# Kernel optimization log

Hardware: AMD Instinct MI355X
Metric: run time of the kernel (lower is better)

## Reference

```python
import jax, jax.numpy as jnp
import numpy as np

DIM = 256      # C
TOPK = 32      # topk_win_num
WIN = 8        # winSize
G = 64         # g (shift group size); 4*G == DIM here


def setup_inputs() -> dict:
    key = jax.random.key(0)
    k0, k1, k2, k3 = jax.random.split(key, 4)
    B, Nt, Ns, C = 32, 256, 4096, DIM
    z = jax.random.normal(k0, (B, Nt, C), jnp.float32)
    x = jax.random.normal(k1, (B, Ns, C), jnp.float32)
    # shift_op_down: Conv2d(C, 4g, 1) -> weight [4g, C]; shift_op_up: Conv2d(4g, C, 1)
    Wd = jax.random.normal(k2, (4 * G, C), jnp.float32) * 0.05
    bd = jnp.zeros((4 * G,), jnp.float32)
    Wu = jax.random.normal(k3, (C, 4 * G), jnp.float32) * 0.05
    bu = jnp.zeros((C,), jnp.float32)
    return {"z": z, "x": x, "Wd": Wd, "bd": bd, "Wu": Wu, "bu": bu}


def reference(z, x, Wd, bd, Wu, bu):
    B, Nt, C = z.shape
    Ns = x.shape[1]
    hs = int(np.sqrt(Ns))
    wn = hs // WIN          # windows per side
    wsa = WIN * WIN         # tokens per window
    K = TOPK

    # AdaptiveMaxPool2d((1,1)) over template tokens -> global max per channel
    z_max = jnp.max(z, axis=1)                               # [B, C]
    sim = jnp.einsum('bc,bnc->bn', z_max, x) / C             # [B, Ns]
    # per-window mean similarity
    sim = sim.reshape(B, wn, WIN, wn, WIN).transpose(0, 1, 3, 2, 4)
    sim = sim.reshape(B, wn * wn, wsa).mean(-1)              # [B, wn*wn]
    idx = jax.lax.top_k(sim, K)[1]                           # [B, K]

    # windowed view of search tokens: [B, wn*wn, wsa, C]
    x_win = x.reshape(B, wn, WIN, wn, WIN, C).transpose(0, 1, 3, 2, 4, 5)
    x_win = x_win.reshape(B, wn * wn, wsa, C)
    x_sel = jnp.take_along_axis(x_win, idx[:, :, None, None], axis=1)  # [B, K, wsa, C]

    xe = x_sel.reshape(B * K, WIN, WIN, C)                   # NHWC per selected window
    t = xe @ Wd.T + bd                                       # 1x1 conv down -> [n, h, w, 4G]

    # 4-direction spatial shift by 1 (zero fill), one channel group per direction
    g0, g1, g2, g3 = t[..., :G], t[..., G:2 * G], t[..., 2 * G:3 * G], t[..., 3 * G:]
    s0 = jnp.pad(g0[:, :, 1:, :], ((0, 0), (0, 0), (0, 1), (0, 0)))  # shift left  (W)
    s1 = jnp.pad(g1[:, :, :-1, :], ((0, 0), (0, 0), (1, 0), (0, 0)))  # shift right (W)
    s2 = jnp.pad(g2[:, 1:, :, :], ((0, 0), (0, 1), (0, 0), (0, 0)))  # shift up    (H)
    s3 = jnp.pad(g3[:, :-1, :, :], ((0, 0), (1, 0), (0, 0), (0, 0)))  # shift down  (H)
    sh = jnp.concatenate([s0, s1, s2, s3], axis=-1)          # [n, h, w, 4G]

    up = sh @ Wu.T + bu                                      # 1x1 conv up -> [n, h, w, C]
    out = (xe + up).reshape(B, K * WIN * WIN, C)             # [B, K*wsa, C]
    return out
```

## Files before the change

kernel.cpp:

```cpp
#include <hip/hip_runtime.h>
#include <hip/hip_bf16.h>

#define C_DIM 256
#define B_SZ 32
#define NS 4096
#define NT_Z 256
#define TOPK_K 32
#define NWIN 64
#define WTOK 64

typedef __attribute__((ext_vector_type(8))) short short8;
typedef __attribute__((ext_vector_type(4))) float f32x4;

static __device__ inline unsigned short f2b(float f) {
  union { float f; unsigned int u; } x; x.f = f;
  unsigned int u = x.u;
  return (unsigned short)((u + 0x7FFFu + ((u >> 16) & 1u)) >> 16);
}
static __device__ inline float b2f(unsigned int h16) {
  union { unsigned int u; float f; } x; x.u = h16 << 16;
  return x.f;
}

__global__ void prep_kernel(const float* __restrict__ Wd, const float* __restrict__ Wu,
                            unsigned short* __restrict__ Wdb, unsigned short* __restrict__ Wub,
                            const float* __restrict__ z, float* __restrict__ zpart) {
  int blk = blockIdx.x;
  if (blk < 64) {
    int i = blk * 256 + threadIdx.x;
    float4 a = ((const float4*)Wd)[i];
    float4 c = ((const float4*)Wu)[i];
    ushort4 ha, hc;
    ha.x = f2b(a.x); ha.y = f2b(a.y); ha.z = f2b(a.z); ha.w = f2b(a.w);
    hc.x = f2b(c.x); hc.y = f2b(c.y); hc.z = f2b(c.z); hc.w = f2b(c.w);
    ((ushort4*)Wdb)[i] = ha;
    ((ushort4*)Wub)[i] = hc;
  } else {
    int i = blk - 64;
    int b = i >> 3, ch = i & 7;
    int c = threadIdx.x;
    const float* p = z + ((size_t)b * NT_Z + ch * 32) * C_DIM + c;
    float m = p[0];
    for (int n = 1; n < 32; ++n) m = fmaxf(m, p[(size_t)n * C_DIM]);
    zpart[(size_t)i * C_DIM + c] = m;
  }
}

__global__ __launch_bounds__(256) void winscore_kernel(const float* __restrict__ x,
                                                       const float* __restrict__ zpart,
                                                       float* __restrict__ score) {
  int b = blockIdx.x >> 6;
  int w = blockIdx.x & 63;
  int wy = w >> 3, wx = w & 7;

  __shared__ float zs[C_DIM];
  {
    float m = zpart[(size_t)(b * 8) * C_DIM + threadIdx.x];
    #pragma unroll
    for (int ch = 1; ch < 8; ++ch)
      m = fmaxf(m, zpart[(size_t)(b * 8 + ch) * C_DIM + threadIdx.x]);
    zs[threadIdx.x] = m;
  }
  __syncthreads();

  int wv = threadIdx.x >> 6;
  int ln = threadIdx.x & 63;

  float a0 = 0.f, a1 = 0.f, a2 = 0.f, a3 = 0.f;
  for (int t = 0; t < 16; ++t) {
    int tok = wv * 16 + t;
    int iy = tok >> 3, ix = tok & 7;
    int n = (wy * 8 + iy) * 64 + wx * 8 + ix;
    const float4 v = *(const float4*)(x + ((size_t)b * NS + n) * C_DIM + ln * 4);
    a0 += v.x; a1 += v.y; a2 += v.z; a3 += v.w;
  }
  const float4 z4 = ((const float4*)zs)[ln];
  float p = a0 * z4.x + a1 * z4.y + a2 * z4.z + a3 * z4.w;
  for (int off = 32; off >= 1; off >>= 1) p += __shfl_xor(p, off);

  __shared__ float wsum[4];
  if (ln == 0) wsum[wv] = p;
  __syncthreads();
  if (threadIdx.x == 0) score[blockIdx.x] = wsum[0] + wsum[1] + wsum[2] + wsum[3];
}

__global__ __launch_bounds__(256, 2) void fused_win(
    const float* __restrict__ x, const float* __restrict__ score,
    const unsigned short* __restrict__ Wdb, const unsigned short* __restrict__ Wub,
    const float* __restrict__ bd, const float* __restrict__ bu,
    float* __restrict__ out)
{
  __shared__ unsigned short xe_s[WTOK * C_DIM];
  __shared__ unsigned short t_s[WTOK * C_DIM];
  __shared__ float sc[NWIN];
  __shared__ int wsel_s;

  const int bk = blockIdx.x;
  const int b = bk >> 5;
  const int kk = bk & 31;
  const int tid = threadIdx.x;

  if (tid < NWIN) sc[tid] = score[b * NWIN + tid];
  __syncthreads();
  if (tid < NWIN) {
    float v = sc[tid];
    int rank = 0;
    #pragma unroll
    for (int j = 0; j < NWIN; ++j) {
      float sj = sc[j];
      rank += (sj > v) || (sj == v && j < tid);
    }
    if (rank == kk) wsel_s = tid;
  }
  __syncthreads();
  const int wsel = wsel_s;
  const int wy = wsel >> 3, wx = wsel & 7;

  const int wv = tid >> 6;
  const int ln = tid & 63;
  const int lr = ln & 15;
  const int lg = ln >> 4;

  const unsigned short* wdbase = Wdb + ((size_t)(wv * 64 + lr)) * C_DIM + lg * 8;
  const unsigned short* wubase = Wub + ((size_t)(wv * 64 + lr)) * C_DIM + lg * 8;

  short8 wreg[8][4];
  #pragma unroll
  for (int ks = 0; ks < 8; ++ks)
    #pragma unroll
    for (int nt = 0; nt < 4; ++nt)
      wreg[ks][nt] = *(const short8*)(wdbase + nt * 16 * C_DIM + ks * 32);

  const int c4 = tid & 63;
  const int m0w = tid >> 6;
  {
    const float* xb = x + (size_t)b * NS * C_DIM + c4 * 4;
    float4 xv[16];
    #pragma unroll
    for (int i = 0; i < 16; ++i) {
      int m = m0w + i * 4;
      int n = (wy * 8 + (m >> 3)) * 64 + wx * 8 + (m & 7);
      xv[i] = *(const float4*)(xb + (size_t)n * C_DIM);
    }
    #pragma unroll
    for (int i = 0; i < 16; ++i) {
      int m = m0w + i * 4;
      ushort4 h;
      h.x = f2b(xv[i].x); h.y = f2b(xv[i].y); h.z = f2b(xv[i].z); h.w = f2b(xv[i].w);
      int byteoff = m * 512 + ((c4 * 8) ^ ((m & 7) << 4));
      *(ushort4*)((char*)xe_s + byteoff) = h;
    }
  }
  __syncthreads();

  f32x4 acc[4][4];
  #pragma unroll
  for (int a = 0; a < 4; ++a)
    #pragma unroll
    for (int n2 = 0; n2 < 4; ++n2) acc[a][n2] = (f32x4){0.f, 0.f, 0.f, 0.f};

  #pragma unroll
  for (int ks = 0; ks < 8; ++ks) {
    const int kb = ks * 64 + lg * 16;
    short8 af[4];
    #pragma unroll
    for (int mt = 0; mt < 4; ++mt) {
      int m = mt * 16 + lr;
      af[mt] = *(const short8*)((const char*)xe_s + m * 512 + (kb ^ ((m & 7) << 4)));
    }
    #pragma unroll
    for (int mt = 0; mt < 4; ++mt)
      #pragma unroll
      for (int nt = 0; nt < 4; ++nt)
        acc[mt][nt] = __builtin_amdgcn_mfma_f32_16x16x32_bf16(af[mt], wreg[ks][nt], acc[mt][nt], 0, 0, 0);
  }

  #pragma unroll
  for (int nt = 0; nt < 4; ++nt) {
    int o = wv * 64 + nt * 16 + lr;
    float bdv = bd[o];
    #pragma unroll
    for (int mt = 0; mt < 4; ++mt) {
      #pragma unroll
      for (int r = 0; r < 4; ++r) {
        int m = mt * 16 + lg * 4 + r;
        float v = acc[mt][nt][r] + bdv;
        *(unsigned short*)((char*)t_s + m * 512 + ((o * 2) ^ ((m & 7) << 4))) = f2b(v);
      }
    }
  }

  short8 wreg2[8][4];
  #pragma unroll
  for (int ks = 0; ks < 8; ++ks)
    #pragma unroll
    for (int nt = 0; nt < 4; ++nt)
      wreg2[ks][nt] = *(const short8*)(wubase + nt * 16 * C_DIM + ks * 32);

  __syncthreads();

  f32x4 acc2[4][4];
  #pragma unroll
  for (int a = 0; a < 4; ++a)
    #pragma unroll
    for (int n2 = 0; n2 < 4; ++n2) acc2[a][n2] = (f32x4){0.f, 0.f, 0.f, 0.f};

  #pragma unroll
  for (int ks = 0; ks < 8; ++ks) {
    const int g = ks >> 1;
    const int dd = ((g & 1) ? -1 : 1) * ((g & 2) ? 8 : 1);
    const int kb = ks * 64 + lg * 16;
    short8 af[4];
    #pragma unroll
    for (int mt = 0; mt < 4; ++mt) {
      int m = mt * 16 + lr;
      int pos = (g & 2) ? (m >> 3) : (m & 7);
      bool ok = (g & 1) ? (pos > 0) : (pos < 7);
      int ms = m + dd;
      ms = ms < 0 ? 0 : (ms > 63 ? 63 : ms);
      short8 v = *(const short8*)((const char*)t_s + ms * 512 + (kb ^ ((ms & 7) << 4)));
      const short8 zed = {0, 0, 0, 0, 0, 0, 0, 0};
      af[mt] = ok ? v : zed;
    }
    #pragma unroll
    for (int mt = 0; mt < 4; ++mt)
      #pragma unroll
      for (int nt = 0; nt < 4; ++nt)
        acc2[mt][nt] = __builtin_amdgcn_mfma_f32_16x16x32_bf16(af[mt], wreg2[ks][nt], acc2[mt][nt], 0, 0, 0);
  }

  __syncthreads();

  #pragma unroll
  for (int nt = 0; nt < 4; ++nt) {
    int c = wv * 64 + nt * 16 + lr;
    #pragma unroll
    for (int mt = 0; mt < 4; ++mt) {
      #pragma unroll
      for (int r = 0; r < 4; ++r) {
        int m = mt * 16 + lg * 4 + r;
        *(unsigned short*)((char*)t_s + m * 512 + ((c * 2) ^ ((m & 7) << 4))) = f2b(acc2[mt][nt][r]);
      }
    }
  }
  __syncthreads();

  {
    const float4 bu4 = *(const float4*)(bu + c4 * 4);
    float* ob = out + (size_t)bk * WTOK * C_DIM + c4 * 4;
    #pragma unroll
    for (int i = 0; i < 16; ++i) {
      int m = m0w + i * 4;
      int off = m * 512 + ((c4 * 8) ^ ((m & 7) << 4));
      ushort4 xe4 = *(const ushort4*)((const char*)xe_s + off);
      ushort4 up4 = *(const ushort4*)((const char*)t_s + off);
      float4 o;
      o.x = b2f(xe4.x) + b2f(up4.x) + bu4.x;
      o.y = b2f(xe4.y) + b2f(up4.y) + bu4.y;
      o.z = b2f(xe4.z) + b2f(up4.z) + bu4.z;
      o.w = b2f(xe4.w) + b2f(up4.w) + bu4.w;
      *(float4*)(ob + (size_t)m * C_DIM) = o;
    }
  }
}

extern "C" void kernel_launch(void* const* d_in, const int* in_sizes, int n_in,
                              void* d_out, int out_size, void* d_ws, size_t ws_size,
                              hipStream_t stream) {
  const float* z  = (const float*)d_in[0];
  const float* x  = (const float*)d_in[1];
  const float* Wd = (const float*)d_in[2];
  const float* bd = (const float*)d_in[3];
  const float* Wu = (const float*)d_in[4];
  const float* bu = (const float*)d_in[5];
  float* out = (float*)d_out;

  char* ws = (char*)d_ws;
  unsigned short* Wdb = (unsigned short*)(ws);
  unsigned short* Wub = (unsigned short*)(ws + 131072);
  float* zpart = (float*)(ws + 262144);
  float* score = (float*)(ws + 524288);

  hipLaunchKernelGGL(prep_kernel, dim3(320), dim3(256), 0, stream, Wd, Wu, Wdb, Wub, z, zpart);
  hipLaunchKernelGGL(winscore_kernel, dim3(B_SZ * NWIN), dim3(256), 0, stream, x, zpart, score);
  hipLaunchKernelGGL(fused_win, dim3(B_SZ * TOPK_K), dim3(256), 0, stream,
                     x, score, Wdb, Wub, bd, bu, out);
}
```

Measured before the change: 81.59 us.

## Split fused window kernel into top-k, down-GEMM and up-GEMM kernels

Splits the single fused kernel into a small top-k kernel and two GEMM kernels, each using one 32KB LDS buffer and streaming weights per k-step instead of holding them all in registers. This is meant to raise occupancy (launch bounds go from 2 to 4 blocks per CU) and remove the duplicated top-k ranking done in every block. The intermediate bf16 activations go through the output buffer in global memory, and the residual x is re-read in fp32 from global memory, so the cost is extra global traffic and two more launches.

```diff
diff --git a/kernel.cpp b/kernel.cpp
--- a/kernel.cpp
+++ b/kernel.cpp
@@ -84,75 +84,65 @@
   if (threadIdx.x == 0) score[blockIdx.x] = wsum[0] + wsum[1] + wsum[2] + wsum[3];
 }
 
-__global__ __launch_bounds__(256, 2) void fused_win(
-    const float* __restrict__ x, const float* __restrict__ score,
-    const unsigned short* __restrict__ Wdb, const unsigned short* __restrict__ Wub,
-    const float* __restrict__ bd, const float* __restrict__ bu,
+__global__ void topk_kernel(const float* __restrict__ score, int* __restrict__ idx) {
+  int b = blockIdx.x;
+  int w = threadIdx.x;
+  __shared__ float s[NWIN];
+  float v = score[b * NWIN + w];
+  s[w] = v;
+  __syncthreads();
+  int rank = 0;
+  for (int j = 0; j < NWIN; ++j) {
+    float sj = s[j];
+    rank += (sj > v) || (sj == v && j < w);
+  }
+  if (rank < TOPK_K) idx[b * TOPK_K + rank] = w;
+}
+
+__global__ __launch_bounds__(256, 4) void gemm1_win(
+    const float* __restrict__ x, const int* __restrict__ idx,
+    const unsigned short* __restrict__ Wdb, const float* __restrict__ bd,
     float* __restrict__ out)
 {
   __shared__ unsigned short xe_s[WTOK * C_DIM];
-  __shared__ unsigned short t_s[WTOK * C_DIM];
-  __shared__ float sc[NWIN];
-  __shared__ int wsel_s;
 
   const int bk = blockIdx.x;
   const int b = bk >> 5;
-  const int kk = bk & 31;
   const int tid = threadIdx.x;
-
-  if (tid < NWIN) sc[tid] = score[b * NWIN + tid];
-  __syncthreads();
-  if (tid < NWIN) {
-    float v = sc[tid];
-    int rank = 0;
-    #pragma unroll
-    for (int j = 0; j < NWIN; ++j) {
-      float sj = sc[j];
-      rank += (sj > v) || (sj == v && j < tid);
-    }
-    if (rank == kk) wsel_s = tid;
-  }
-  __syncthreads();
-  const int wsel = wsel_s;
+  const int wsel = idx[bk];
   const int wy = wsel >> 3, wx = wsel & 7;
 
   const int wv = tid >> 6;
   const int ln = tid & 63;
   const int lr = ln & 15;
   const int lg = ln >> 4;
-
-  const unsigned short* wdbase = Wdb + ((size_t)(wv * 64 + lr)) * C_DIM + lg * 8;
-  const unsigned short* wubase = Wub + ((size_t)(wv * 64 + lr)) * C_DIM + lg * 8;
-
-  short8 wreg[8][4];
-  #pragma unroll
-  for (int ks = 0; ks < 8; ++ks)
-    #pragma unroll
-    for (int nt = 0; nt < 4; ++nt)
-      wreg[ks][nt] = *(const short8*)(wdbase + nt * 16 * C_DIM + ks * 32);
-
   const int c4 = tid & 63;
   const int m0w = tid >> 6;
+
   {
     const float* xb = x + (size_t)b * NS * C_DIM + c4 * 4;
-    float4 xv[16];
-    #pragma unroll
-    for (int i = 0; i < 16; ++i) {
-      int m = m0w + i * 4;
-      int n = (wy * 8 + (m >> 3)) * 64 + wx * 8 + (m & 7);
-      xv[i] = *(const float4*)(xb + (size_t)n * C_DIM);
-    }
-    #pragma unroll
-    for (int i = 0; i < 16; ++i) {
-      int m = m0w + i * 4;
-      ushort4 h;
-      h.x = f2b(xv[i].x); h.y = f2b(xv[i].y); h.z = f2b(xv[i].z); h.w = f2b(xv[i].w);
-      int byteoff = m * 512 + ((c4 * 8) ^ ((m & 7) << 4));
-      *(ushort4*)((char*)xe_s + byteoff) = h;
-    }
-  }
-  __syncthreads();
-
+    #pragma unroll
+    for (int h = 0; h < 2; ++h) {
+      float4 xv[8];
+      #pragma unroll
+      for (int i = 0; i < 8; ++i) {
+        int m = m0w + (h * 8 + i) * 4;
+        int n = (wy * 8 + (m >> 3)) * 64 + wx * 8 + (m & 7);
+        xv[i] = *(const float4*)(xb + (size_t)n * C_DIM);
+      }
+      #pragma unroll
+      for (int i = 0; i < 8; ++i) {
+        int m = m0w + (h * 8 + i) * 4;
+        ushort4 hs;
+        hs.x = f2b(xv[i].x); hs.y = f2b(xv[i].y); hs.z = f2b(xv[i].z); hs.w = f2b(xv[i].w);
+        int byteoff = m * 512 + ((c4 * 8) ^ ((m & 7) << 4));
+        *(ushort4*)((char*)xe_s + byteoff) = hs;
+      }
+    }
+  }
+  __syncthreads();
+
+  const unsigned short* wdbase = Wdb + (size_t)(wv * 64 + lr) * C_DIM + lg * 8;
   f32x4 acc[4][4];
   #pragma unroll
   for (int a = 0; a < 4; ++a)
@@ -161,6 +151,10 @@
 
   #pragma unroll
   for (int ks = 0; ks < 8; ++ks) {
+    short8 bf[4];
+    #pragma unroll
+    for (int nt = 0; nt < 4; ++nt)
+      bf[nt] = *(const short8*)(wdbase + nt * 16 * C_DIM + ks * 32);
     const int kb = ks * 64 + lg * 16;
     short8 af[4];
     #pragma unroll
@@ -172,8 +166,9 @@
     for (int mt = 0; mt < 4; ++mt)
       #pragma unroll
       for (int nt = 0; nt < 4; ++nt)
-        acc[mt][nt] = __builtin_amdgcn_mfma_f32_16x16x32_bf16(af[mt], wreg[ks][nt], acc[mt][nt], 0, 0, 0);
-  }
+        acc[mt][nt] = __builtin_amdgcn_mfma_f32_16x16x32_bf16(af[mt], bf[nt], acc[mt][nt], 0, 0, 0);
+  }
+  __syncthreads();
 
   #pragma unroll
   for (int nt = 0; nt < 4; ++nt) {
@@ -184,29 +179,69 @@
       #pragma unroll
       for (int r = 0; r < 4; ++r) {
         int m = mt * 16 + lg * 4 + r;
-        float v = acc[mt][nt][r] + bdv;
-        *(unsigned short*)((char*)t_s + m * 512 + ((o * 2) ^ ((m & 7) << 4))) = f2b(v);
+        *(unsigned short*)((char*)xe_s + m * 512 + ((o * 2) ^ ((m & 7) << 4))) = f2b(acc[mt][nt][r] + bdv);
       }
     }
   }
-
-  short8 wreg2[8][4];
-  #pragma unroll
-  for (int ks = 0; ks < 8; ++ks)
+  __syncthreads();
+
+  {
+    char* tb = (char*)out + (size_t)bk * 65536 + 32768;
+    #pragma unroll
+    for (int i = 0; i < 16; ++i) {
+      int m = m0w + i * 4;
+      ushort4 v = *(const ushort4*)((const char*)xe_s + m * 512 + ((c4 * 8) ^ ((m & 7) << 4)));
+      *(ushort4*)(tb + m * 512 + c4 * 8) = v;
+    }
+  }
+}
+
+__global__ __launch_bounds__(256, 4) void gemm2_win(
+    const float* __restrict__ x, const int* __restrict__ idx,
+    const unsigned short* __restrict__ Wub, const float* __restrict__ bu,
+    float* __restrict__ out)
+{
+  __shared__ unsigned short t_s[WTOK * C_DIM];
+
+  const int bk = blockIdx.x;
+  const int b = bk >> 5;
+  const int tid = threadIdx.x;
+  const int wsel = idx[bk];
+  const int wy = wsel >> 3, wx = wsel & 7;
+
+  const int wv = tid >> 6;
+  const int ln = tid & 63;
+  const int lr = ln & 15;
+  const int lg = ln >> 4;
+  const int c4 = tid & 63;
+  const int m0w = tid >> 6;
+
+  {
+    const char* tb = (const char*)out + (size_t)bk * 65536 + 32768;
+    const int r0 = tid >> 5;
+    const int c8 = tid & 31;
+    #pragma unroll
+    for (int j = 0; j < 8; ++j) {
+      int r = r0 + j * 8;
+      short8 v = *(const short8*)(tb + r * 512 + c8 * 16);
+      *(short8*)((char*)t_s + r * 512 + ((c8 * 16) ^ ((r & 7) << 4))) = v;
+    }
+  }
+  __syncthreads();
+
+  const unsigned short* wubase = Wub + (size_t)(wv * 64 + lr) * C_DIM + lg * 8;
+  f32x4 acc2[4][4];
+  #pragma unroll
+  for (int a = 0; a < 4; ++a)
+    #pragma unroll
+    for (int n2 = 0; n2 < 4; ++n2) acc2[a][n2] = (f32x4){0.f, 0.f, 0.f, 0.f};
+
+  #pragma unroll
+  for (int ks = 0; ks < 8; ++ks) {
+    short8 bf[4];
     #pragma unroll
     for (int nt = 0; nt < 4; ++nt)
-      wreg2[ks][nt] = *(const short8*)(wubase + nt * 16 * C_DIM + ks * 32);
-
-  __syncthreads();
-
-  f32x4 acc2[4][4];
-  #pragma unroll
-  for (int a = 0; a < 4; ++a)
-    #pragma unroll
-    for (int n2 = 0; n2 < 4; ++n2) acc2[a][n2] = (f32x4){0.f, 0.f, 0.f, 0.f};
-
-  #pragma unroll
-  for (int ks = 0; ks < 8; ++ks) {
+      bf[nt] = *(const short8*)(wubase + nt * 16 * C_DIM + ks * 32);
     const int g = ks >> 1;
     const int dd = ((g & 1) ? -1 : 1) * ((g & 2) ? 8 : 1);
     const int kb = ks * 64 + lg * 16;
@@ -226,9 +261,8 @@
     for (int mt = 0; mt < 4; ++mt)
       #pragma unroll
       for (int nt = 0; nt < 4; ++nt)
-        acc2[mt][nt] = __builtin_amdgcn_mfma_f32_16x16x32_bf16(af[mt], wreg2[ks][nt], acc2[mt][nt], 0, 0, 0);
-  }
-
+        acc2[mt][nt] = __builtin_amdgcn_mfma_f32_16x16x32_bf16(af[mt], bf[nt], acc2[mt][nt], 0, 0, 0);
+  }
   __syncthreads();
 
   #pragma unroll
@@ -247,18 +281,19 @@
 
   {
     const float4 bu4 = *(const float4*)(bu + c4 * 4);
+    const float* xb = x + (size_t)b * NS * C_DIM + c4 * 4;
     float* ob = out + (size_t)bk * WTOK * C_DIM + c4 * 4;
     #pragma unroll
     for (int i = 0; i < 16; ++i) {
       int m = m0w + i * 4;
-      int off = m * 512 + ((c4 * 8) ^ ((m & 7) << 4));
-      ushort4 xe4 = *(const ushort4*)((const char*)xe_s + off);
-      ushort4 up4 = *(const ushort4*)((const char*)t_s + off);
+      int n = (wy * 8 + (m >> 3)) * 64 + wx * 8 + (m & 7);
+      float4 xr = *(const float4*)(xb + (size_t)n * C_DIM);
+      ushort4 u4 = *(const ushort4*)((const char*)t_s + m * 512 + ((c4 * 8) ^ ((m & 7) << 4)));
       float4 o;
-      o.x = b2f(xe4.x) + b2f(up4.x) + bu4.x;
-      o.y = b2f(xe4.y) + b2f(up4.y) + bu4.y;
-      o.z = b2f(xe4.z) + b2f(up4.z) + bu4.z;
-      o.w = b2f(xe4.w) + b2f(up4.w) + bu4.w;
+      o.x = xr.x + b2f(u4.x) + bu4.x;
+      o.y = xr.y + b2f(u4.y) + bu4.y;
+      o.z = xr.z + b2f(u4.z) + bu4.z;
+      o.w = xr.w + b2f(u4.w) + bu4.w;
       *(float4*)(ob + (size_t)m * C_DIM) = o;
     }
   }
@@ -280,9 +315,11 @@
   unsigned short* Wub = (unsigned short*)(ws + 131072);
   float* zpart = (float*)(ws + 262144);
   float* score = (float*)(ws + 524288);
+  int*   idx   = (int*)(ws + 532480);
 
   hipLaunchKernelGGL(prep_kernel, dim3(320), dim3(256), 0, stream, Wd, Wu, Wdb, Wub, z, zpart);
   hipLaunchKernelGGL(winscore_kernel, dim3(B_SZ * NWIN), dim3(256), 0, stream, x, zpart, score);
-  hipLaunchKernelGGL(fused_win, dim3(B_SZ * TOPK_K), dim3(256), 0, stream,
-                     x, score, Wdb, Wub, bd, bu, out);
-}
+  hipLaunchKernelGGL(topk_kernel, dim3(B_SZ), dim3(NWIN), 0, stream, score, idx);
+  hipLaunchKernelGGL(gemm1_win, dim3(B_SZ * TOPK_K), dim3(256), 0, stream, x, idx, Wdb, bd, out);
+  hipLaunchKernelGGL(gemm2_win, dim3(B_SZ * TOPK_K), dim3(256), 0, stream, x, idx, Wub, bu, out);
+}
```

Result: slower. 108.8 us (+33.4%).

## Process two selected windows per block and prefetch the second window's input

Applied to the files above, without the earlier changes.

Each block of fused_win now handles two consecutive top-k windows instead of one, which halves the grid to 512 blocks. The second window's x tile is loaded into registers during the first window's up-projection, so its global load latency overlaps with compute. The ranking work is shared across both windows. The cost is lower block-level parallelism, since 512 blocks on 256 CUs with 2 blocks per CU may leave units underused. Register pressure also rises from the extra 16 float4 prefetch buffer, and the weight fragments are reloaded for the second window.

```diff
diff --git a/kernel.cpp b/kernel.cpp
--- a/kernel.cpp
+++ b/kernel.cpp
@@ -93,11 +93,11 @@
   __shared__ unsigned short xe_s[WTOK * C_DIM];
   __shared__ unsigned short t_s[WTOK * C_DIM];
   __shared__ float sc[NWIN];
-  __shared__ int wsel_s;
+  __shared__ int wsel2_s[2];
 
   const int bk = blockIdx.x;
-  const int b = bk >> 5;
-  const int kk = bk & 31;
+  const int b = bk >> 4;
+  const int kk0 = (bk & 15) * 2;
   const int tid = threadIdx.x;
 
   if (tid < NWIN) sc[tid] = score[b * NWIN + tid];
@@ -110,19 +110,26 @@
       float sj = sc[j];
       rank += (sj > v) || (sj == v && j < tid);
     }
-    if (rank == kk) wsel_s = tid;
-  }
-  __syncthreads();
-  const int wsel = wsel_s;
-  const int wy = wsel >> 3, wx = wsel & 7;
+    int rr = rank - kk0;
+    if (rr >= 0 && rr < 2) wsel2_s[rr] = tid;
+  }
+  __syncthreads();
 
   const int wv = tid >> 6;
   const int ln = tid & 63;
   const int lr = ln & 15;
   const int lg = ln >> 4;
+  const int c4 = tid & 63;
+  const int m0w = tid >> 6;
 
   const unsigned short* wdbase = Wdb + ((size_t)(wv * 64 + lr)) * C_DIM + lg * 8;
   const unsigned short* wubase = Wub + ((size_t)(wv * 64 + lr)) * C_DIM + lg * 8;
+  const float* xb = x + (size_t)b * NS * C_DIM + c4 * 4;
+
+  const int wsel0 = wsel2_s[0];
+  const int wy0 = wsel0 >> 3, wx0 = wsel0 & 7;
+  const int wsel1 = wsel2_s[1];
+  const int wy1 = wsel1 >> 3, wx1 = wsel1 & 7;
 
   short8 wreg[8][4];
   #pragma unroll
@@ -131,15 +138,12 @@
     for (int nt = 0; nt < 4; ++nt)
       wreg[ks][nt] = *(const short8*)(wdbase + nt * 16 * C_DIM + ks * 32);
 
-  const int c4 = tid & 63;
-  const int m0w = tid >> 6;
   {
-    const float* xb = x + (size_t)b * NS * C_DIM + c4 * 4;
     float4 xv[16];
     #pragma unroll
     for (int i = 0; i < 16; ++i) {
       int m = m0w + i * 4;
-      int n = (wy * 8 + (m >> 3)) * 64 + wx * 8 + (m & 7);
+      int n = (wy0 * 8 + (m >> 3)) * 64 + wx0 * 8 + (m & 7);
       xv[i] = *(const float4*)(xb + (size_t)n * C_DIM);
     }
     #pragma unroll
@@ -229,6 +233,14 @@
         acc2[mt][nt] = __builtin_amdgcn_mfma_f32_16x16x32_bf16(af[mt], wreg2[ks][nt], acc2[mt][nt], 0, 0, 0);
   }
 
+  float4 xv1[16];
+  #pragma unroll
+  for (int i = 0; i < 16; ++i) {
+    int m = m0w + i * 4;
+    int n = (wy1 * 8 + (m >> 3)) * 64 + wx1 * 8 + (m & 7);
+    xv1[i] = *(const float4*)(xb + (size_t)n * C_DIM);
+  }
+
   __syncthreads();
 
   #pragma unroll
@@ -247,7 +259,7 @@
 
   {
     const float4 bu4 = *(const float4*)(bu + c4 * 4);
-    float* ob = out + (size_t)bk * WTOK * C_DIM + c4 * 4;
+    float* ob = out + (size_t)(b * 32 + kk0) * WTOK * C_DIM + c4 * 4;
     #pragma unroll
     for (int i = 0; i < 16; ++i) {
       int m = m0w + i * 4;
@@ -262,6 +274,129 @@
       *(float4*)(ob + (size_t)m * C_DIM) = o;
     }
   }
+  __syncthreads();
+
+  #pragma unroll
+  for (int ks = 0; ks < 8; ++ks)
+    #pragma unroll
+    for (int nt = 0; nt < 4; ++nt)
+      wreg[ks][nt] = *(const short8*)(wdbase + nt * 16 * C_DIM + ks * 32);
+
+  #pragma unroll
+  for (int i = 0; i < 16; ++i) {
+    int m = m0w + i * 4;
+    ushort4 h;
+    h.x = f2b(xv1[i].x); h.y = f2b(xv1[i].y); h.z = f2b(xv1[i].z); h.w = f2b(xv1[i].w);
+    int byteoff = m * 512 + ((c4 * 8) ^ ((m & 7) << 4));
+    *(ushort4*)((char*)xe_s + byteoff) = h;
+  }
+  __syncthreads();
+
+  #pragma unroll
+  for (int a = 0; a < 4; ++a)
+    #pragma unroll
+    for (int n2 = 0; n2 < 4; ++n2) acc[a][n2] = (f32x4){0.f, 0.f, 0.f, 0.f};
+
+  #pragma unroll
+  for (int ks = 0; ks < 8; ++ks) {
+    const int kb = ks * 64 + lg * 16;
+    short8 af[4];
+    #pragma unroll
+    for (int mt = 0; mt < 4; ++mt) {
+      int m = mt * 16 + lr;
+      af[mt] = *(const short8*)((const char*)xe_s + m * 512 + (kb ^ ((m & 7) << 4)));
+    }
+    #pragma unroll
+    for (int mt = 0; mt < 4; ++mt)
+      #pragma unroll
+      for (int nt = 0; nt < 4; ++nt)
+        acc[mt][nt] = __builtin_amdgcn_mfma_f32_16x16x32_bf16(af[mt], wreg[ks][nt], acc[mt][nt], 0, 0, 0);
+  }
+
+  #pragma unroll
+  for (int nt = 0; nt < 4; ++nt) {
+    int o = wv * 64 + nt * 16 + lr;
+    float bdv = bd[o];
+    #pragma unroll
+    for (int mt = 0; mt < 4; ++mt) {
+      #pragma unroll
+      for (int r = 0; r < 4; ++r) {
+        int m = mt * 16 + lg * 4 + r;
+        float v = acc[mt][nt][r] + bdv;
+        *(unsigned short*)((char*)t_s + m * 512 + ((o * 2) ^ ((m & 7) << 4))) = f2b(v);
+      }
+    }
+  }
+
+  #pragma unroll
+  for (int ks = 0; ks < 8; ++ks)
+    #pragma unroll
+    for (int nt = 0; nt < 4; ++nt)
+      wreg2[ks][nt] = *(const short8*)(wubase + nt * 16 * C_DIM + ks * 32);
+
+  __syncthreads();
+
+  #pragma unroll
+  for (int a = 0; a < 4; ++a)
+    #pragma unroll
+    for (int n2 = 0; n2 < 4; ++n2) acc2[a][n2] = (f32x4){0.f, 0.f, 0.f, 0.f};
+
+  #pragma unroll
+  for (int ks = 0; ks < 8; ++ks) {
+    const int g = ks >> 1;
+    const int dd = ((g & 1) ? -1 : 1) * ((g & 2) ? 8 : 1);
+    const int kb = ks * 64 + lg * 16;
+    short8 af[4];
+    #pragma unroll
+    for (int mt = 0; mt < 4; ++mt) {
+      int m = mt * 16 + lr;
+      int pos = (g & 2) ? (m >> 3) : (m & 7);
+      bool ok = (g & 1) ? (pos > 0) : (pos < 7);
+      int ms = m + dd;
+      ms = ms < 0 ? 0 : (ms > 63 ? 63 : ms);
+      short8 v = *(const short8*)((const char*)t_s + ms * 512 + (kb ^ ((ms & 7) << 4)));
+      const short8 zed = {0, 0, 0, 0, 0, 0, 0, 0};
+      af[mt] = ok ? v : zed;
+    }
+    #pragma unroll
+    for (int mt = 0; mt < 4; ++mt)
+      #pragma unroll
+      for (int nt = 0; nt < 4; ++nt)
+        acc2[mt][nt] = __builtin_amdgcn_mfma_f32_16x16x32_bf16(af[mt], wreg2[ks][nt], acc2[mt][nt], 0, 0, 0);
+  }
+  __syncthreads();
+
+  #pragma unroll
+  for (int nt = 0; nt < 4; ++nt) {
+    int c = wv * 64 + nt * 16 + lr;
+    #pragma unroll
+    for (int mt = 0; mt < 4; ++mt) {
+      #pragma unroll
+      for (int r = 0; r < 4; ++r) {
+        int m = mt * 16 + lg * 4 + r;
+        *(unsigned short*)((char*)t_s + m * 512 + ((c * 2) ^ ((m & 7) << 4))) = f2b(acc2[mt][nt][r]);
+      }
+    }
+  }
+  __syncthreads();
+
+  {
+    const float4 bu4 = *(const float4*)(bu + c4 * 4);
+    float* ob = out + (size_t)(b * 32 + kk0 + 1) * WTOK * C_DIM + c4 * 4;
+    #pragma unroll
+    for (int i = 0; i < 16; ++i) {
+      int m = m0w + i * 4;
+      int off = m * 512 + ((c4 * 8) ^ ((m & 7) << 4));
+      ushort4 xe4 = *(const ushort4*)((const char*)xe_s + off);
+      ushort4 up4 = *(const ushort4*)((const char*)t_s + off);
+      float4 o;
+      o.x = b2f(xe4.x) + b2f(up4.x) + bu4.x;
+      o.y = b2f(xe4.y) + b2f(up4.y) + bu4.y;
+      o.z = b2f(xe4.z) + b2f(up4.z) + bu4.z;
+      o.w = b2f(xe4.w) + b2f(up4.w) + bu4.w;
+      *(float4*)(ob + (size_t)m * C_DIM) = o;
+    }
+  }
 }
 
 extern "C" void kernel_launch(void* const* d_in, const int* in_sizes, int n_in,
@@ -283,6 +418,6 @@
 
   hipLaunchKernelGGL(prep_kernel, dim3(320), dim3(256), 0, stream, Wd, Wu, Wdb, Wub, z, zpart);
   hipLaunchKernelGGL(winscore_kernel, dim3(B_SZ * NWIN), dim3(256), 0, stream, x, zpart, score);
-  hipLaunchKernelGGL(fused_win, dim3(B_SZ * TOPK_K), dim3(256), 0, stream,
+  hipLaunchKernelGGL(fused_win, dim3(B_SZ * TOPK_K / 2), dim3(256), 0, stream,
                      x, score, Wdb, Wub, bd, bu, out);
 }
```

Result: slower. 129.8 us (+59.1%).
